# Performance work log

Measured on AMD Instinct MI355X. Metric: run time of the kernel, lower is better.

## Reference

```python
import jax, jax.numpy as jnp
import numpy as np

E, H = 1024, 16


def setup_inputs() -> dict:
    key = jax.random.key(0)
    k1, k2, k3, k4 = jax.random.split(key, 4)
    B, L = 4, 2048
    embeddings = jax.random.normal(k1, (B, L, E), dtype=jnp.float32)
    mask = jax.random.randint(k2, (B, L, L), 0, 2) == 1  # True = masked out
    # Params (torch Linear y = x @ W.T; we store already-transposed [in, out])
    W_qkv = jax.random.normal(k3, (E, 3 * E), dtype=jnp.float32) * 0.02
    W_out = jax.random.normal(k4, (E, E), dtype=jnp.float32) * 0.02
    return {"embeddings": embeddings, "mask": mask, "W_qkv": W_qkv, "W_out": W_out}


def reference(embeddings, mask, W_qkv, W_out):
    B, L, E_ = embeddings.shape
    A = E_ // H
    scale = A ** (-0.5)
    qkv = embeddings @ W_qkv                       # [B, L, 3E]
    qkv = qkv.reshape(B, L, H, 3 * A).transpose(0, 2, 1, 3)  # [B, H, L, 3A]
    q, k, v = jnp.split(qkv, 3, axis=-1)           # each [B, H, L, A]
    scores = jnp.einsum('bhqa,bhka->bhqk', q, k) * scale  # [B, H, L, L]
    m = mask[:, None, :, :]                        # [B, 1, L, L]
    fully = jnp.all(m, axis=-1, keepdims=True)     # rows with every key masked
    scores = jnp.where(m, -jnp.inf, scores)
    scores = jnp.where(fully, 0.0, scores)         # keep softmax finite
    attn = jax.nn.softmax(scores, axis=-1)
    attn = jnp.where(fully, 0.0, attn)             # == torch nan_to_num(0)
    values = jnp.einsum('bhqk,bhka->bhqa', attn, v)  # [B, H, L, A]
    values = values.transpose(0, 2, 1, 3).reshape(B, L, E_)
    return values @ W_out
```

## Files before the change

### kernel.cpp

```cpp
#include <hip/hip_runtime.h>
#include <hip/hip_bf16.h>

#define B_   4
#define L_   2048
#define E_   1024
#define H_   16
#define T_   8192
#define K_   1024

typedef __attribute__((ext_vector_type(8))) short bf16x8;
typedef __attribute__((ext_vector_type(4))) float f32x4;

#define CSC_ (0.125f * 1.44269504f)

__device__ __forceinline__ ushort f2b(float f) {
    union { float f; unsigned u; } x; x.f = f;
    unsigned r = (x.u + 0x7fffu + ((x.u >> 16) & 1u)) >> 16;
    return (ushort)r;
}

__device__ __forceinline__ unsigned pack2bf(float a, float b) {
#if __has_builtin(__builtin_amdgcn_cvt_pk_bf16_f32)
    auto t = __builtin_amdgcn_cvt_pk_bf16_f32(a, b);
    return __builtin_bit_cast(unsigned, t);
#else
    return (unsigned)f2b(a) | ((unsigned)f2b(b) << 16);
#endif
}

#define GLD_LDS16(gp, lp) __builtin_amdgcn_global_load_lds( \
    (const __attribute__((address_space(1))) void*)(gp), \
    (__attribute__((address_space(3))) void*)(lp), 16, 0, 0)

__global__ void detect_mask_layout(const unsigned char* __restrict__ m, int* flag) {
    __shared__ int s;
    if (threadIdx.x == 0) s = 0;
    __syncthreads();
    int found = 0;
    for (int i = threadIdx.x; i < 4096; i += 256)
        if ((i & 3) != 0 && m[i] != 0) found = 1;
    if (found) atomicOr(&s, 1);
    __syncthreads();
    if (threadIdx.x == 0) *flag = s;
}

__global__ void pack_mask(const void* __restrict__ mraw, const int* __restrict__ flag,
                          unsigned long long* __restrict__ bits) {
    int row  = blockIdx.x;
    int lane = threadIdx.x & 63;
    int wave = threadIdx.x >> 6;
    int isByte = *flag;
    const unsigned char* mb = (const unsigned char*)mraw;
    const int*           mi = (const int*)mraw;
    long long base = (long long)row * L_;
    for (int w = wave; w < 32; w += 4) {
        int idx = w * 64 + lane;
        int v = isByte ? (int)mb[base + idx] : mi[base + idx];
        unsigned long long word = __ballot(v == 0);
        if (lane == 0) bits[row * 32 + w] = word;
    }
}

__global__ __launch_bounds__(256) void conv_bf16(const float* __restrict__ in,
                                                 ushort* __restrict__ out) {
    int i = blockIdx.x * 256 + threadIdx.x;
    float4 v = ((const float4*)in)[i];
    uint2 o;
    o.x = pack2bf(v.x, v.y);
    o.y = pack2bf(v.z, v.w);
    ((uint2*)out)[i] = o;
}

__global__ __launch_bounds__(256) void transpose_conv(const float* __restrict__ in,
        ushort* __restrict__ out, int R, int Cn) {
    __shared__ float t[32][33];
    int c0 = blockIdx.x * 32, r0 = blockIdx.y * 32;
    int x = threadIdx.x & 31, y = threadIdx.x >> 5;
#pragma unroll
    for (int k = 0; k < 4; ++k)
        t[y + k * 8][x] = in[(size_t)(r0 + y + k * 8) * Cn + c0 + x];
    __syncthreads();
#pragma unroll
    for (int k = 0; k < 4; ++k)
        out[(size_t)(c0 + y + k * 8) * R + r0 + x] = f2b(t[x][y + k * 8]);
}

template<int NDIM, int MODE>
__global__ __launch_bounds__(256) void gemm_bf16(
        const ushort* __restrict__ Ab, const ushort* __restrict__ Bt,
        float* __restrict__ Cg, ushort* __restrict__ Qb,
        ushort* __restrict__ Kb, ushort* __restrict__ Vt) {
    __shared__ ushort As[128 * 64];
    __shared__ ushort Bs[128 * 64];
    const int tid = threadIdx.x;
    const int wv = tid >> 6, ln = tid & 63;
    const int bn = blockIdx.x * 128, bm = blockIdx.y * 128;
    const int wm = (wv & 1) * 64, wn = (wv >> 1) * 64;
    const int row16 = ln & 15, quad = ln >> 4;
    const int cg8 = (((ln & 7) ^ (ln >> 3)) * 8);

    f32x4 acc[4][4];
#pragma unroll
    for (int i = 0; i < 4; ++i)
#pragma unroll
        for (int j = 0; j < 4; ++j) acc[i][j] = (f32x4){0.f, 0.f, 0.f, 0.f};

    for (int k0 = 0; k0 < K_; k0 += 64) {
        __syncthreads();
#pragma unroll
        for (int it = 0; it < 4; ++it) {
            int rA = wv * 32 + it * 8 + (ln >> 3);
            GLD_LDS16(Ab + (size_t)(bm + rA) * K_ + k0 + cg8, &As[(wv * 32 + it * 8) * 64]);
            GLD_LDS16(Bt + (size_t)(bn + rA) * K_ + k0 + cg8, &Bs[(wv * 32 + it * 8) * 64]);
        }
        __syncthreads();
#pragma unroll
        for (int ks = 0; ks < 2; ++ks) {
            const int ch = (((ks * 4 + quad) ^ (ln & 7)) * 8);
            bf16x8 af[4], bf[4];
#pragma unroll
            for (int i = 0; i < 4; ++i)
                af[i] = *(const bf16x8*)&As[(wm + i * 16 + row16) * 64 + ch];
#pragma unroll
            for (int j = 0; j < 4; ++j)
                bf[j] = *(const bf16x8*)&Bs[(wn + j * 16 + row16) * 64 + ch];
#pragma unroll
            for (int i = 0; i < 4; ++i)
#pragma unroll
                for (int j = 0; j < 4; ++j)
                    acc[i][j] = __builtin_amdgcn_mfma_f32_16x16x32_bf16(
                        af[i], bf[j], acc[i][j], 0, 0, 0);
        }
    }

    if (MODE == 0) {
#pragma unroll
        for (int i = 0; i < 4; ++i)
#pragma unroll
            for (int j = 0; j < 4; ++j) {
                int col = bn + wn + j * 16 + row16;
#pragma unroll
                for (int r = 0; r < 4; ++r) {
                    int row = bm + wm + i * 16 + quad * 4 + r;
                    Cg[(size_t)row * NDIM + col] = acc[i][j][r];
                }
            }
    } else {
#pragma unroll
        for (int j = 0; j < 4; ++j) {
            int col = bn + wn + j * 16 + row16;
            int h = col / 192, w = col - h * 192;
            int sel = w >> 6, a = w & 63;
            float qs = (sel == 0) ? CSC_ : 1.0f;
#pragma unroll
            for (int i = 0; i < 4; ++i)
#pragma unroll
                for (int r = 0; r < 4; ++r) {
                    int rowg = bm + wm + i * 16 + quad * 4 + r;
                    int b = rowg >> 11, l = rowg & 2047;
                    ushort v = f2b(acc[i][j][r] * qs);
                    size_t bh = (size_t)(b * H_ + h);
                    if (sel == 0)      Qb[(bh * L_ + l) * 64 + a] = v;
                    else if (sel == 1) Kb[(bh * L_ + l) * 64 + a] = v;
                    else               Vt[(bh * 64 + a) * L_ + l] = v;
                }
        }
    }
}

__global__ __launch_bounds__(256) void attn_mfma(
        const ushort* __restrict__ Qb, const ushort* __restrict__ Kb,
        const ushort* __restrict__ Vt, const unsigned long long* __restrict__ bits,
        ushort* __restrict__ vals) {
    __shared__ ushort Ks[64 * 64];
    __shared__ ushort Vs[64 * 64];
    __shared__ ushort PQ[64 * 64];

    const int tid = threadIdx.x, wv = tid >> 6, ln = tid & 63;
    const int bh = blockIdx.y, b = bh >> 4, h = bh & 15;
    const int q0 = blockIdx.x * 64;
    const int row16 = ln & 15, quad = ln >> 4;
    const int cg8 = (((ln & 7) ^ (ln >> 3)) * 8);

    {
        const ushort* Qg = Qb + ((size_t)bh * L_ + q0) * 64;
#pragma unroll
        for (int it = 0; it < 2; ++it) {
            GLD_LDS16(Qg + (size_t)(wv * 16 + it * 8 + (ln >> 3)) * 64 + cg8,
                      &PQ[(wv * 16 + it * 8) * 64]);
        }
    }
    __syncthreads();

    const int ch0 = ((quad ^ (ln & 7)) * 8);
    const int ch1 = (((4 + quad) ^ (ln & 7)) * 8);
    bf16x8 aq[2];
    aq[0] = *(const bf16x8*)&PQ[(wv * 16 + row16) * 64 + ch0];
    aq[1] = *(const bf16x8*)&PQ[(wv * 16 + row16) * 64 + ch1];
    ushort* Pw = &PQ[wv * 1024];

    bf16x8 vone;
#pragma unroll
    for (int i = 0; i < 8; ++i) vone[i] = (short)0x3F80;

    f32x4 oacc[4], lacc;
#pragma unroll
    for (int t = 0; t < 4; ++t) oacc[t] = (f32x4){0.f, 0.f, 0.f, 0.f};
    lacc = (f32x4){0.f, 0.f, 0.f, 0.f};

    const unsigned long long* bpp =
        bits + ((size_t)b * L_ + q0 + wv * 16 + quad * 4) * 32;

    const ushort* Kg = Kb + (size_t)bh * L_ * 64;
    const ushort* Vg = Vt + (size_t)bh * 64 * L_;
    const int rh = row16 >> 3, rl = row16 & 7;
    const int pxb = (quad * 4) & 7;

    for (int kt = 0; kt < 32; ++kt) {
        __syncthreads();
#pragma unroll
        for (int it = 0; it < 2; ++it) {
            int r = wv * 16 + it * 8 + (ln >> 3);
            GLD_LDS16(Kg + (size_t)(kt * 64 + r) * 64 + cg8, &Ks[(wv * 16 + it * 8) * 64]);
            GLD_LDS16(Vg + (size_t)r * L_ + kt * 64 + cg8,   &Vs[(wv * 16 + it * 8) * 64]);
        }
        unsigned long long wm0 = bpp[kt], wm1 = bpp[kt + 32],
                           wm2 = bpp[kt + 64], wm3 = bpp[kt + 96];
        __syncthreads();

        f32x4 sa[4];
#pragma unroll
        for (int t = 0; t < 4; ++t) sa[t] = (f32x4){0.f, 0.f, 0.f, 0.f};
#pragma unroll
        for (int t = 0; t < 4; ++t) {
            bf16x8 bk0 = *(const bf16x8*)&Ks[(t * 16 + row16) * 64 + ch0];
            sa[t] = __builtin_amdgcn_mfma_f32_16x16x32_bf16(aq[0], bk0, sa[t], 0, 0, 0);
            bf16x8 bk1 = *(const bf16x8*)&Ks[(t * 16 + row16) * 64 + ch1];
            sa[t] = __builtin_amdgcn_mfma_f32_16x16x32_bf16(aq[1], bk1, sa[t], 0, 0, 0);
        }

        unsigned long long wmv[4] = {wm0, wm1, wm2, wm3};
#pragma unroll
        for (int r = 0; r < 4; ++r) {
            unsigned long long sh = wmv[r] >> row16;
            unsigned lo = (unsigned)sh, hi = (unsigned)(sh >> 32);
            unsigned pk01 = pack2bf(exp2f(sa[0][r]), exp2f(sa[1][r]));
            unsigned pk23 = pack2bf(exp2f(sa[2][r]), exp2f(sa[3][r]));
            pk01 &= (lo & 0x00010001u) * 0xFFFFu;
            pk23 &= (hi & 0x00010001u) * 0xFFFFu;
            ushort* pr = Pw + (quad * 4 + r) * 64;
            int px = pxb + r;
            pr[((0 + rh) ^ px) * 8 + rl] = (ushort)pk01;
            pr[((2 + rh) ^ px) * 8 + rl] = (ushort)(pk01 >> 16);
            pr[((4 + rh) ^ px) * 8 + rl] = (ushort)pk23;
            pr[((6 + rh) ^ px) * 8 + rl] = (ushort)(pk23 >> 16);
        }

        {
            bf16x8 ap0 = *(const bf16x8*)&Pw[row16 * 64 + ch0];
            lacc = __builtin_amdgcn_mfma_f32_16x16x32_bf16(ap0, vone, lacc, 0, 0, 0);
#pragma unroll
            for (int t = 0; t < 4; ++t) {
                bf16x8 bv = *(const bf16x8*)&Vs[(t * 16 + row16) * 64 + ch0];
                oacc[t] = __builtin_amdgcn_mfma_f32_16x16x32_bf16(ap0, bv, oacc[t], 0, 0, 0);
            }
            bf16x8 ap1 = *(const bf16x8*)&Pw[row16 * 64 + ch1];
            lacc = __builtin_amdgcn_mfma_f32_16x16x32_bf16(ap1, vone, lacc, 0, 0, 0);
#pragma unroll
            for (int t = 0; t < 4; ++t) {
                bf16x8 bv = *(const bf16x8*)&Vs[(t * 16 + row16) * 64 + ch1];
                oacc[t] = __builtin_amdgcn_mfma_f32_16x16x32_bf16(ap1, bv, oacc[t], 0, 0, 0);
            }
        }
    }

#pragma unroll
    for (int r = 0; r < 4; ++r) {
        float l = lacc[r];
        float inv = (l > 0.f) ? 1.0f / l : 0.f;
        int qrow = q0 + wv * 16 + quad * 4 + r;
        size_t base = ((size_t)b * L_ + qrow) * E_ + h * 64;
#pragma unroll
        for (int t = 0; t < 4; ++t)
            vals[base + t * 16 + row16] = f2b(oacc[t][r] * inv);
    }
}

extern "C" void kernel_launch(void* const* d_in, const int* in_sizes, int n_in,
                              void* d_out, int out_size, void* d_ws, size_t ws_size,
                              hipStream_t stream) {
    const float* emb  = (const float*)d_in[0];
    const void*  mask = d_in[1];
    const float* wqkv = (const float*)d_in[2];
    const float* wout = (const float*)d_in[3];
    float* out = (float*)d_out;

    char* ws = (char*)d_ws;
    const size_t NEED = 4096ull + 2097152ull + 2ull * 46137344ull;
    if (ws_size < NEED) return;

    int* flag = (int*)ws;
    unsigned long long* bits = (unsigned long long*)(ws + 4096);
    ushort* embb  = (ushort*)(ws + 4096 + 2097152);
    ushort* Wqkvt = embb  + 8388608;
    ushort* Wott  = Wqkvt + 3145728;
    ushort* Qb    = Wott  + 1048576;
    ushort* Kb    = Qb    + 8388608;
    ushort* Vt    = Kb    + 8388608;
    ushort* vals  = Vt    + 8388608;

    detect_mask_layout<<<1, 256, 0, stream>>>((const unsigned char*)mask, flag);
    pack_mask<<<T_, 256, 0, stream>>>(mask, flag, bits);
    conv_bf16<<<8192, 256, 0, stream>>>(emb, embb);
    transpose_conv<<<dim3(96, 32), 256, 0, stream>>>(wqkv, Wqkvt, 1024, 3072);
    transpose_conv<<<dim3(32, 32), 256, 0, stream>>>(wout, Wott, 1024, 1024);
    gemm_bf16<3072, 1><<<dim3(24, 64), 256, 0, stream>>>(
        embb, Wqkvt, nullptr, Qb, Kb, Vt);
    attn_mfma<<<dim3(32, 64), 256, 0, stream>>>(Qb, Kb, Vt, bits, vals);
    gemm_bf16<1024, 0><<<dim3(8, 64), 256, 0, stream>>>(
        vals, Wott, out, nullptr, nullptr, nullptr);
}
```

Before: 425.1 us.

## Double-buffer K/V tiles in attention, widen query rows per wave, permute V layout

The attention kernel now gives each wave 32 query rows (128 per block) and walks 32-key tiles. K and V tiles are double-buffered in LDS, so the next tile's global-to-LDS load overlaps the current compute and one barrier per iteration is dropped. V is stored with a permuted key order inside each 32-key group, which lets the P tile be written as packed 32-bit stores into a padded row layout instead of scattered 16-bit swizzled stores. The kernel also switches to the raw hardware exp2 builtin and a cheaper bf16 packing fallback. The trade-off is fewer blocks (half the grid), more registers per wave, and rounding in the fallback pack that is not round-to-nearest-even.

```diff
diff --git a/kernel.cpp b/kernel.cpp
--- a/kernel.cpp
+++ b/kernel.cpp
@@ -19,12 +19,22 @@
     return (ushort)r;
 }
 
+__device__ __forceinline__ float fexp2(float x) {
+#if __has_builtin(__builtin_amdgcn_exp2f)
+    return __builtin_amdgcn_exp2f(x);
+#else
+    return __expf(x * 0.69314718056f);
+#endif
+}
+
 __device__ __forceinline__ unsigned pack2bf(float a, float b) {
 #if __has_builtin(__builtin_amdgcn_cvt_pk_bf16_f32)
     auto t = __builtin_amdgcn_cvt_pk_bf16_f32(a, b);
     return __builtin_bit_cast(unsigned, t);
 #else
-    return (unsigned)f2b(a) | ((unsigned)f2b(b) << 16);
+    unsigned ua = __builtin_bit_cast(unsigned, a) + 0x8000u;
+    unsigned ub = __builtin_bit_cast(unsigned, b) + 0x8000u;
+    return __builtin_amdgcn_perm(ub, ua, 0x07060302);
 #endif
 }
 
@@ -66,8 +76,8 @@
     int i = blockIdx.x * 256 + threadIdx.x;
     float4 v = ((const float4*)in)[i];
     uint2 o;
-    o.x = pack2bf(v.x, v.y);
-    o.y = pack2bf(v.z, v.w);
+    o.x = (unsigned)f2b(v.x) | ((unsigned)f2b(v.y) << 16);
+    o.y = (unsigned)f2b(v.z) | ((unsigned)f2b(v.w) << 16);
     ((uint2*)out)[i] = o;
 }
 
@@ -162,7 +172,11 @@
                     size_t bh = (size_t)(b * H_ + h);
                     if (sel == 0)      Qb[(bh * L_ + l) * 64 + a] = v;
                     else if (sel == 1) Kb[(bh * L_ + l) * 64 + a] = v;
-                    else               Vt[(bh * 64 + a) * L_ + l] = v;
+                    else {
+                        int k5 = l & 31;
+                        int lp = (l & ~31) | (2 * (k5 & 15) + (k5 >> 4));
+                        Vt[(bh * 64 + a) * L_ + lp] = v;
+                    }
                 }
         }
     }
@@ -170,120 +184,133 @@
 
 __global__ __launch_bounds__(256) void attn_mfma(
         const ushort* __restrict__ Qb, const ushort* __restrict__ Kb,
-        const ushort* __restrict__ Vt, const unsigned long long* __restrict__ bits,
+        const ushort* __restrict__ Vt, const unsigned* __restrict__ bits32,
         ushort* __restrict__ vals) {
-    __shared__ ushort Ks[64 * 64];
-    __shared__ ushort Vs[64 * 64];
-    __shared__ ushort PQ[64 * 64];
+    __shared__ ushort Kd[2][32 * 64];
+    __shared__ ushort Vd[2][64 * 32];
+    __shared__ ushort PQ[4][2048];
 
     const int tid = threadIdx.x, wv = tid >> 6, ln = tid & 63;
     const int bh = blockIdx.y, b = bh >> 4, h = bh & 15;
-    const int q0 = blockIdx.x * 64;
+    const int q0 = blockIdx.x * 128;
     const int row16 = ln & 15, quad = ln >> 4;
     const int cg8 = (((ln & 7) ^ (ln >> 3)) * 8);
 
-    {
-        const ushort* Qg = Qb + ((size_t)bh * L_ + q0) * 64;
-#pragma unroll
-        for (int it = 0; it < 2; ++it) {
-            GLD_LDS16(Qg + (size_t)(wv * 16 + it * 8 + (ln >> 3)) * 64 + cg8,
-                      &PQ[(wv * 16 + it * 8) * 64]);
-        }
-    }
-    __syncthreads();
-
-    const int ch0 = ((quad ^ (ln & 7)) * 8);
-    const int ch1 = (((4 + quad) ^ (ln & 7)) * 8);
-    bf16x8 aq[2];
-    aq[0] = *(const bf16x8*)&PQ[(wv * 16 + row16) * 64 + ch0];
-    aq[1] = *(const bf16x8*)&PQ[(wv * 16 + row16) * 64 + ch1];
-    ushort* Pw = &PQ[wv * 1024];
-
-    bf16x8 vone;
-#pragma unroll
-    for (int i = 0; i < 8; ++i) vone[i] = (short)0x3F80;
-
-    f32x4 oacc[4], lacc;
-#pragma unroll
-    for (int t = 0; t < 4; ++t) oacc[t] = (f32x4){0.f, 0.f, 0.f, 0.f};
-    lacc = (f32x4){0.f, 0.f, 0.f, 0.f};
-
-    const unsigned long long* bpp =
-        bits + ((size_t)b * L_ + q0 + wv * 16 + quad * 4) * 32;
-
     const ushort* Kg = Kb + (size_t)bh * L_ * 64;
     const ushort* Vg = Vt + (size_t)bh * 64 * L_;
-    const int rh = row16 >> 3, rl = row16 & 7;
-    const int pxb = (quad * 4) & 7;
-
-    for (int kt = 0; kt < 32; ++kt) {
+    ushort* Qw = &PQ[wv][0];
+
+    {
+        const ushort* Qgw = Qb + ((size_t)bh * L_ + q0 + wv * 32) * 64;
+#pragma unroll
+        for (int it = 0; it < 4; ++it)
+            GLD_LDS16(Qgw + (size_t)(it * 8 + (ln >> 3)) * 64 + cg8, Qw + it * 8 * 64);
+        GLD_LDS16(Kg + (size_t)(wv * 8 + (ln >> 3)) * 64 + cg8, &Kd[0][(wv * 8) * 64]);
+        GLD_LDS16(Vg + (size_t)(wv * 16 + (ln >> 2)) * L_ + (ln & 3) * 8,
+                  &Vd[0][(wv * 16) * 32]);
+    }
+    __syncthreads();
+
+    bf16x8 aq[2][2];
+#pragma unroll
+    for (int rg = 0; rg < 2; ++rg)
+#pragma unroll
+        for (int ks = 0; ks < 2; ++ks) {
+            int row = rg * 16 + row16;
+            aq[rg][ks] = *(const bf16x8*)&Qw[row * 64 + (((ks * 4 + quad) ^ (row & 7)) * 8)];
+        }
+    ushort* Pw = Qw;
+
+    bf16x8 vone;
+#pragma unroll
+    for (int i = 0; i < 8; ++i) vone[i] = (short)0x3F80;
+
+    f32x4 oacc[2][4], lacc[2];
+#pragma unroll
+    for (int rg = 0; rg < 2; ++rg) {
+        lacc[rg] = (f32x4){0.f, 0.f, 0.f, 0.f};
+#pragma unroll
+        for (int t = 0; t < 4; ++t) oacc[rg][t] = (f32x4){0.f, 0.f, 0.f, 0.f};
+    }
+
+    const unsigned* mp0 = bits32 + ((size_t)b * L_ + q0 + wv * 32 + quad * 4) * 64;
+    const unsigned* mp1 = mp0 + 16 * 64;
+
+    for (int kt = 0; kt < 64; ++kt) {
+        const int cur = kt & 1;
         __syncthreads();
-#pragma unroll
-        for (int it = 0; it < 2; ++it) {
-            int r = wv * 16 + it * 8 + (ln >> 3);
-            GLD_LDS16(Kg + (size_t)(kt * 64 + r) * 64 + cg8, &Ks[(wv * 16 + it * 8) * 64]);
-            GLD_LDS16(Vg + (size_t)r * L_ + kt * 64 + cg8,   &Vs[(wv * 16 + it * 8) * 64]);
-        }
-        unsigned long long wm0 = bpp[kt], wm1 = bpp[kt + 32],
-                           wm2 = bpp[kt + 64], wm3 = bpp[kt + 96];
-        __syncthreads();
-
-        f32x4 sa[4];
-#pragma unroll
-        for (int t = 0; t < 4; ++t) sa[t] = (f32x4){0.f, 0.f, 0.f, 0.f};
-#pragma unroll
-        for (int t = 0; t < 4; ++t) {
-            bf16x8 bk0 = *(const bf16x8*)&Ks[(t * 16 + row16) * 64 + ch0];
-            sa[t] = __builtin_amdgcn_mfma_f32_16x16x32_bf16(aq[0], bk0, sa[t], 0, 0, 0);
-            bf16x8 bk1 = *(const bf16x8*)&Ks[(t * 16 + row16) * 64 + ch1];
-            sa[t] = __builtin_amdgcn_mfma_f32_16x16x32_bf16(aq[1], bk1, sa[t], 0, 0, 0);
-        }
-
-        unsigned long long wmv[4] = {wm0, wm1, wm2, wm3};
+        if (kt + 1 < 64) {
+            const int nxt = cur ^ 1;
+            GLD_LDS16(Kg + (size_t)((kt + 1) * 32 + wv * 8 + (ln >> 3)) * 64 + cg8,
+                      &Kd[nxt][(wv * 8) * 64]);
+            GLD_LDS16(Vg + (size_t)(wv * 16 + (ln >> 2)) * L_ + (kt + 1) * 32 + (ln & 3) * 8,
+                      &Vd[nxt][(wv * 16) * 32]);
+        }
+        unsigned w0[4], w1[4];
+#pragma unroll
+        for (int r = 0; r < 4; ++r) { w0[r] = mp0[r * 64 + kt]; w1[r] = mp1[r * 64 + kt]; }
+
+        f32x4 sa[2][2];
+#pragma unroll
+        for (int rg = 0; rg < 2; ++rg)
+#pragma unroll
+            for (int t = 0; t < 2; ++t) sa[rg][t] = (f32x4){0.f, 0.f, 0.f, 0.f};
+#pragma unroll
+        for (int ks = 0; ks < 2; ++ks) {
+            bf16x8 bk[2];
+#pragma unroll
+            for (int t = 0; t < 2; ++t)
+                bk[t] = *(const bf16x8*)&Kd[cur][(t * 16 + row16) * 64 +
+                                                 (((ks * 4 + quad) ^ (row16 & 7)) * 8)];
+#pragma unroll
+            for (int rg = 0; rg < 2; ++rg)
+#pragma unroll
+                for (int t = 0; t < 2; ++t)
+                    sa[rg][t] = __builtin_amdgcn_mfma_f32_16x16x32_bf16(
+                        aq[rg][ks], bk[t], sa[rg][t], 0, 0, 0);
+        }
+
+#pragma unroll
+        for (int rg = 0; rg < 2; ++rg) {
+            const unsigned* wr = rg ? w1 : w0;
+#pragma unroll
+            for (int r = 0; r < 4; ++r) {
+                unsigned sh = wr[r] >> row16;
+                unsigned pk = pack2bf(fexp2(sa[rg][0][r]), fexp2(sa[rg][1][r]));
+                pk &= (sh & 0x00010001u) * 0xFFFFu;
+                *(unsigned*)&Pw[(rg * 16 + quad * 4 + r) * 36 + 2 * row16] = pk;
+            }
+        }
+
+        {
+            bf16x8 bv[4];
+#pragma unroll
+            for (int t = 0; t < 4; ++t)
+                bv[t] = *(const bf16x8*)&Vd[cur][(t * 16 + row16) * 32 + quad * 8];
+#pragma unroll
+            for (int rg = 0; rg < 2; ++rg) {
+                bf16x8 ap = *(const bf16x8*)&Pw[(rg * 16 + row16) * 36 + quad * 8];
+                lacc[rg] = __builtin_amdgcn_mfma_f32_16x16x32_bf16(ap, vone, lacc[rg], 0, 0, 0);
+#pragma unroll
+                for (int t = 0; t < 4; ++t)
+                    oacc[rg][t] = __builtin_amdgcn_mfma_f32_16x16x32_bf16(
+                        ap, bv[t], oacc[rg][t], 0, 0, 0);
+            }
+        }
+    }
+
+#pragma unroll
+    for (int rg = 0; rg < 2; ++rg)
 #pragma unroll
         for (int r = 0; r < 4; ++r) {
-            unsigned long long sh = wmv[r] >> row16;
-            unsigned lo = (unsigned)sh, hi = (unsigned)(sh >> 32);
-            unsigned pk01 = pack2bf(exp2f(sa[0][r]), exp2f(sa[1][r]));
-            unsigned pk23 = pack2bf(exp2f(sa[2][r]), exp2f(sa[3][r]));
-            pk01 &= (lo & 0x00010001u) * 0xFFFFu;
-            pk23 &= (hi & 0x00010001u) * 0xFFFFu;
-            ushort* pr = Pw + (quad * 4 + r) * 64;
-            int px = pxb + r;
-            pr[((0 + rh) ^ px) * 8 + rl] = (ushort)pk01;
-            pr[((2 + rh) ^ px) * 8 + rl] = (ushort)(pk01 >> 16);
-            pr[((4 + rh) ^ px) * 8 + rl] = (ushort)pk23;
-            pr[((6 + rh) ^ px) * 8 + rl] = (ushort)(pk23 >> 16);
-        }
-
-        {
-            bf16x8 ap0 = *(const bf16x8*)&Pw[row16 * 64 + ch0];
-            lacc = __builtin_amdgcn_mfma_f32_16x16x32_bf16(ap0, vone, lacc, 0, 0, 0);
-#pragma unroll
-            for (int t = 0; t < 4; ++t) {
-                bf16x8 bv = *(const bf16x8*)&Vs[(t * 16 + row16) * 64 + ch0];
-                oacc[t] = __builtin_amdgcn_mfma_f32_16x16x32_bf16(ap0, bv, oacc[t], 0, 0, 0);
-            }
-            bf16x8 ap1 = *(const bf16x8*)&Pw[row16 * 64 + ch1];
-            lacc = __builtin_amdgcn_mfma_f32_16x16x32_bf16(ap1, vone, lacc, 0, 0, 0);
-#pragma unroll
-            for (int t = 0; t < 4; ++t) {
-                bf16x8 bv = *(const bf16x8*)&Vs[(t * 16 + row16) * 64 + ch1];
-                oacc[t] = __builtin_amdgcn_mfma_f32_16x16x32_bf16(ap1, bv, oacc[t], 0, 0, 0);
-            }
-        }
-    }
-
-#pragma unroll
-    for (int r = 0; r < 4; ++r) {
-        float l = lacc[r];
-        float inv = (l > 0.f) ? 1.0f / l : 0.f;
-        int qrow = q0 + wv * 16 + quad * 4 + r;
-        size_t base = ((size_t)b * L_ + qrow) * E_ + h * 64;
-#pragma unroll
-        for (int t = 0; t < 4; ++t)
-            vals[base + t * 16 + row16] = f2b(oacc[t][r] * inv);
-    }
+            float l = lacc[rg][r];
+            float inv = (l > 0.f) ? 1.0f / l : 0.f;
+            int qrow = q0 + wv * 32 + rg * 16 + quad * 4 + r;
+            size_t base = ((size_t)b * L_ + qrow) * E_ + h * 64;
+#pragma unroll
+            for (int t = 0; t < 4; ++t)
+                vals[base + t * 16 + row16] = f2b(oacc[rg][t][r] * inv);
+        }
 }
 
 extern "C" void kernel_launch(void* const* d_in, const int* in_sizes, int n_in,
@@ -316,7 +343,8 @@
     transpose_conv<<<dim3(32, 32), 256, 0, stream>>>(wout, Wott, 1024, 1024);
     gemm_bf16<3072, 1><<<dim3(24, 64), 256, 0, stream>>>(
         embb, Wqkvt, nullptr, Qb, Kb, Vt);
-    attn_mfma<<<dim3(32, 64), 256, 0, stream>>>(Qb, Kb, Vt, bits, vals);
+    attn_mfma<<<dim3(16, 64), 256, 0, stream>>>(
+        Qb, Kb, Vt, (const unsigned*)bits, vals);
     gemm_bf16<1024, 0><<<dim3(8, 64), 256, 0, stream>>>(
         vals, Wott, out, nullptr, nullptr, nullptr);
 }
```

Result: slower. 451.8 us (+6.3%).
